# Kernel tuning notes

Hardware: AMD Instinct MI355X
Metric: run time of the kernel (lower is better)

Reference implementation:

```python
import jax, jax.numpy as jnp
import numpy as np

B, N, D = 4, 4096, 512
H = 8
HD = D // H  # 64


def setup_inputs() -> dict:
    key = jax.random.key(0)
    ks = jax.random.split(key, 9)
    s = 1.0 / np.sqrt(D)
    return {
        "x": jax.random.normal(ks[0], (B, N, D), dtype=jnp.float32),
        "Wq": jax.random.normal(ks[1], (D, D), dtype=jnp.float32) * s,
        "bq": jax.random.normal(ks[2], (D,), dtype=jnp.float32) * 0.01,
        "Wk": jax.random.normal(ks[3], (D, D), dtype=jnp.float32) * s,
        "bk": jax.random.normal(ks[4], (D,), dtype=jnp.float32) * 0.01,
        "Wv": jax.random.normal(ks[5], (D, D), dtype=jnp.float32) * s,
        "bv": jax.random.normal(ks[6], (D,), dtype=jnp.float32) * 0.01,
        "Wo": jax.random.normal(ks[7], (D, D), dtype=jnp.float32) * s,
        "bo": jax.random.normal(ks[8], (D,), dtype=jnp.float32) * 0.01,
    }


def reference(x, Wq, bq, Wk, bk, Wv, bv, Wo, bo):
    # projections -> [B, H, N, HD]
    def split_heads(t):
        return t.reshape(B, N, H, HD).transpose(0, 2, 1, 3)

    q = split_heads(x @ Wq.T + bq)
    k = split_heads(x @ Wk.T + bk)
    v = split_heads(x @ Wv.T + bv)

    scale = 1.0 / np.sqrt(HD).astype(np.float32)
    scores = jnp.einsum("bhqd,bhkd->bhqk", q, k) * scale  # [B,H,N,N]
    attn = jax.nn.softmax(scores, axis=-1)
    out = jnp.einsum("bhqk,bhkd->bhqd", attn, v)  # [B,H,N,HD]
    out = out.transpose(0, 2, 1, 3).reshape(B, N, D)
    return out @ Wo.T + bo
```

## Files before the change

kernel.cpp:

```cpp
#include <hip/hip_runtime.h>
#include <hip/hip_bf16.h>

#define BB 4
#define NN 4096
#define DD 512
#define HH 8
#define HD 64

typedef __attribute__((ext_vector_type(4))) float f32x4;
typedef __attribute__((ext_vector_type(16))) float f32x16;
typedef __attribute__((ext_vector_type(8))) short short8;
typedef __attribute__((ext_vector_type(4))) unsigned int uint4v;

static __device__ __forceinline__ unsigned short f2bf(float f) {
    unsigned int u = __float_as_uint(f);
    u += 0x7fff + ((u >> 16) & 1);
    return (unsigned short)(u >> 16);
}

__global__ void convert_bf16(const float* __restrict__ in,
                             unsigned short* __restrict__ out, int n) {
    int i = (blockIdx.x * blockDim.x + threadIdx.x) * 8;
    int stride = gridDim.x * blockDim.x * 8;
    for (; i + 7 < n; i += stride) {
        f32x4 a = *reinterpret_cast<const f32x4*>(in + i);
        f32x4 b = *reinterpret_cast<const f32x4*>(in + i + 4);
        short8 o;
        o[0] = (short)f2bf(a[0]); o[1] = (short)f2bf(a[1]);
        o[2] = (short)f2bf(a[2]); o[3] = (short)f2bf(a[3]);
        o[4] = (short)f2bf(b[0]); o[5] = (short)f2bf(b[1]);
        o[6] = (short)f2bf(b[2]); o[7] = (short)f2bf(b[3]);
        *reinterpret_cast<short8*>(out + i) = o;
    }
}

__global__ void convert_weights(const float* __restrict__ W0, const float* __restrict__ W1,
                                const float* __restrict__ W2, const float* __restrict__ W3,
                                unsigned short* __restrict__ out) {
    int which = blockIdx.x >> 7;
    const float* src = which == 0 ? W0 : which == 1 ? W1 : which == 2 ? W2 : W3;
    unsigned short* dst = out + (size_t)which * DD * DD;
    int i = ((blockIdx.x & 127) * blockDim.x + threadIdx.x) * 8;
    f32x4 a = *reinterpret_cast<const f32x4*>(src + i);
    f32x4 b = *reinterpret_cast<const f32x4*>(src + i + 4);
    short8 o;
    o[0] = (short)f2bf(a[0]); o[1] = (short)f2bf(a[1]);
    o[2] = (short)f2bf(a[2]); o[3] = (short)f2bf(a[3]);
    o[4] = (short)f2bf(b[0]); o[5] = (short)f2bf(b[1]);
    o[6] = (short)f2bf(b[2]); o[7] = (short)f2bf(b[3]);
    *reinterpret_cast<short8*>(dst + i) = o;
}

template <int OUT_BF16>
__global__ __launch_bounds__(256)
void gemm_bias(const unsigned short* __restrict__ A,
               const unsigned short* __restrict__ W,
               const float* __restrict__ bias,
               void* __restrict__ Cout, float scale) {
    __shared__ uint4 ldsA[128 * 4];
    __shared__ uint4 ldsB[128 * 4];
    const int t = threadIdx.x;
    const int lane = t & 63;
    const int w = t >> 6;
    const int wr = w >> 1, wc = w & 1;
    const int brow = (int)blockIdx.y * 128;
    const int bcol = (int)blockIdx.x * 128;
    const int l16 = lane & 15;
    const int lq = lane >> 4;

    f32x4 acc[4][4] = {};

    const int sr = t >> 1;
    const int c16 = (t & 1) * 2;

    for (int k0 = 0; k0 < 512; k0 += 32) {
        const uint4* gA = reinterpret_cast<const uint4*>(A + (size_t)(brow + sr) * 512 + k0 + c16 * 8);
        const uint4* gB = reinterpret_cast<const uint4*>(W + (size_t)(bcol + sr) * 512 + k0 + c16 * 8);
        uint4 a0 = gA[0], a1 = gA[1];
        uint4 b0 = gB[0], b1 = gB[1];
        __syncthreads();
        ldsA[(sr * 4 + c16) ^ (sr & 7)]     = a0;
        ldsA[(sr * 4 + c16 + 1) ^ (sr & 7)] = a1;
        ldsB[(sr * 4 + c16) ^ (sr & 7)]     = b0;
        ldsB[(sr * 4 + c16 + 1) ^ (sr & 7)] = b1;
        __syncthreads();
        short8 af[4], bfr[4];
#pragma unroll
        for (int m = 0; m < 4; ++m) {
            int ra = wr * 64 + m * 16 + l16;
            af[m] = *reinterpret_cast<short8*>(&ldsA[(ra * 4 + lq) ^ (ra & 7)]);
            int rb = wc * 64 + m * 16 + l16;
            bfr[m] = *reinterpret_cast<short8*>(&ldsB[(rb * 4 + lq) ^ (rb & 7)]);
        }
#pragma unroll
        for (int m = 0; m < 4; ++m)
#pragma unroll
            for (int n = 0; n < 4; ++n)
                acc[m][n] = __builtin_amdgcn_mfma_f32_16x16x32_bf16(af[m], bfr[n], acc[m][n], 0, 0, 0);
    }

#pragma unroll
    for (int m = 0; m < 4; ++m) {
        int row = brow + wr * 64 + m * 16 + lq * 4;
#pragma unroll
        for (int n = 0; n < 4; ++n) {
            int col = bcol + wc * 64 + n * 16 + l16;
            float bv = bias[col];
#pragma unroll
            for (int r = 0; r < 4; ++r) {
                float v = (acc[m][n][r] + bv) * scale;
                if (OUT_BF16) {
                    ((unsigned short*)Cout)[(size_t)(row + r) * 512 + col] = f2bf(v);
                } else {
                    ((float*)Cout)[(size_t)(row + r) * 512 + col] = v;
                }
            }
        }
    }
}

__global__ __launch_bounds__(256)
void transpose_v(const unsigned short* __restrict__ Vb, unsigned short* __restrict__ Vt) {
    __shared__ unsigned short tile[64][72];
    const int bh = blockIdx.y;
    const int b = bh >> 3, h = bh & 7;
    const int n0 = blockIdx.x * 64;
    const int t = threadIdx.x;
    {
        int r = t >> 2;
        int cs = (t & 3) * 16;
        const short8* src = reinterpret_cast<const short8*>(
            Vb + (size_t)(b * NN + n0 + r) * DD + h * HD + cs);
        short8 v0 = src[0], v1 = src[1];
#pragma unroll
        for (int j = 0; j < 8; ++j) {
            tile[r][cs + j]     = (unsigned short)v0[j];
            tile[r][cs + 8 + j] = (unsigned short)v1[j];
        }
    }
    __syncthreads();
    {
        int d = t >> 2;
        int ns = (t & 3) * 16;
        short8 o0, o1;
#pragma unroll
        for (int j = 0; j < 8; ++j) {
            o0[j] = (short)tile[ns + j][d];
            o1[j] = (short)tile[ns + 8 + j][d];
        }
        unsigned short* dst = Vt + ((size_t)bh * HD + d) * NN + n0 + ns;
        *reinterpret_cast<short8*>(dst)     = o0;
        *reinterpret_cast<short8*>(dst + 8) = o1;
    }
}

__global__ __launch_bounds__(256, 3)
void flash_attn(const unsigned short* __restrict__ Qb,
                const unsigned short* __restrict__ Kb,
                const unsigned short* __restrict__ Vt,
                unsigned short* __restrict__ Ob) {
    __shared__ __align__(16) char lds[32768];
    const int t = threadIdx.x;
    const int lane = t & 63;
    const int w = t >> 6;
    const int nid = (blockIdx.x & 7) * 128 + (blockIdx.x >> 3);
    const int bh = nid >> 5;
    const int qb = nid & 31;
    const int b = bh >> 3, h = bh & 7;
    const int q0 = qb * 128 + w * 32;
    const int l32 = lane & 31;
    const int hi = lane >> 5;

    const int i8 = lane >> 3, g8 = lane & 7;

    const unsigned short* qptr = Qb + (size_t)(b * NN + q0 + l32) * DD + h * HD + hi * 8;
    short8 qf[4];
#pragma unroll
    for (int c = 0; c < 4; ++c)
        qf[c] = *reinterpret_cast<const short8*>(qptr + c * 16);

    const f32x16 Z = {};
    f32x16 OT0 = {}, OT1 = {};
    float lsx = 0.f, lsy = 0.f;

    int koff[8], voff[8];
#pragma unroll
    for (int sub = 0; sub < 2; ++sub) {
#pragma unroll
        for (int c = 0; c < 4; ++c) {
            int row = sub * 32 + l32;
            int g = (hi + 2 * c) ^ (row & 7) ^ ((row >> 3) & 7);
            koff[sub * 4 + c] = row * 128 + g * 16;
        }
#pragma unroll
        for (int dblk = 0; dblk < 2; ++dblk)
#pragma unroll
            for (int c2 = 0; c2 < 2; ++c2) {
                int row = dblk * 32 + l32;
                int g = ((sub << 2) + (c2 << 1) + hi) ^ (row & 7) ^ ((row >> 3) & 7);
                voff[sub * 4 + dblk * 2 + c2] = 8192 + row * 128 + g * 16;
            }
    }

    const int rowl0 = w * 16 + i8;
    const int rowl1 = w * 16 + 8 + i8;
    const int gs0 = (g8 ^ i8 ^ ((2 * w) & 7)) * 8;
    const int gs1 = (g8 ^ i8 ^ ((2 * w + 1) & 7)) * 8;
    const unsigned short* kp0 = Kb + (size_t)(b * NN + rowl0) * DD + h * HD + gs0;
    const unsigned short* kp1 = Kb + (size_t)(b * NN + rowl1) * DD + h * HD + gs1;
    const unsigned short* vp0 = Vt + ((size_t)bh * HD + rowl0) * NN + gs0;
    const unsigned short* vp1 = Vt + ((size_t)bh * HD + rowl1) * NN + gs1;

    auto STAGE = [&](int bb) {
        __builtin_amdgcn_global_load_lds(
            (const __attribute__((address_space(1))) void*)kp0,
            (__attribute__((address_space(3))) void*)(lds + bb + (w * 16) * 128), 16, 0, 0);
        __builtin_amdgcn_global_load_lds(
            (const __attribute__((address_space(1))) void*)kp1,
            (__attribute__((address_space(3))) void*)(lds + bb + (w * 16 + 8) * 128), 16, 0, 0);
        __builtin_amdgcn_global_load_lds(
            (const __attribute__((address_space(1))) void*)vp0,
            (__attribute__((address_space(3))) void*)(lds + bb + 8192 + (w * 16) * 128), 16, 0, 0);
        __builtin_amdgcn_global_load_lds(
            (const __attribute__((address_space(1))) void*)vp1,
            (__attribute__((address_space(3))) void*)(lds + bb + 8192 + (w * 16 + 8) * 128), 16, 0, 0);
        kp0 += 64 * DD; kp1 += 64 * DD; vp0 += 64; vp1 += 64;
    };

    auto softpack = [&](const f32x16& S, short8& pa, short8& pb) {
        unsigned int wq[8];
#pragma unroll
        for (int j = 0; j < 8; ++j) {
            float p0 = __builtin_exp2f(S[2 * j]);
            float p1 = __builtin_exp2f(S[2 * j + 1]);
            lsx += p0; lsy += p1;
            asm("v_cvt_pk_bf16_f32 %0, %1, %2" : "=v"(wq[j]) : "v"(p0), "v"(p1));
        }
        asm("v_permlane32_swap_b32 %0, %1" : "+v"(wq[0]), "+v"(wq[2]));
        asm("v_permlane32_swap_b32 %0, %1" : "+v"(wq[1]), "+v"(wq[3]));
        asm("v_permlane32_swap_b32 %0, %1" : "+v"(wq[4]), "+v"(wq[6]));
        asm("v_permlane32_swap_b32 %0, %1" : "+v"(wq[5]), "+v"(wq[7]));
        uint4v pu0 = {wq[0], wq[1], wq[2], wq[3]};
        uint4v pu1 = {wq[4], wq[5], wq[6], wq[7]};
        pa = __builtin_bit_cast(short8, pu0);
        pb = __builtin_bit_cast(short8, pu1);
    };

    auto COMPUTE = [&](int BO) {
        short8 kf0, kf1, kf2, kf3;
        kf0 = *reinterpret_cast<const short8*>(lds + BO + koff[0]);
        kf1 = *reinterpret_cast<const short8*>(lds + BO + koff[1]);
        kf2 = *reinterpret_cast<const short8*>(lds + BO + koff[2]);
        kf3 = *reinterpret_cast<const short8*>(lds + BO + koff[3]);
        f32x16 S;
        __builtin_amdgcn_s_setprio(1);
        S = __builtin_amdgcn_mfma_f32_32x32x16_bf16(kf0, qf[0], Z, 0, 0, 0);
        S = __builtin_amdgcn_mfma_f32_32x32x16_bf16(kf1, qf[1], S, 0, 0, 0);
        S = __builtin_amdgcn_mfma_f32_32x32x16_bf16(kf2, qf[2], S, 0, 0, 0);
        S = __builtin_amdgcn_mfma_f32_32x32x16_bf16(kf3, qf[3], S, 0, 0, 0);
        __builtin_amdgcn_s_setprio(0);
        short8 vf0 = *reinterpret_cast<const short8*>(lds + BO + voff[0]);
        short8 vf1 = *reinterpret_cast<const short8*>(lds + BO + voff[1]);
        short8 vf2 = *reinterpret_cast<const short8*>(lds + BO + voff[2]);
        short8 vf3 = *reinterpret_cast<const short8*>(lds + BO + voff[3]);
        kf0 = *reinterpret_cast<const short8*>(lds + BO + koff[4]);
        kf1 = *reinterpret_cast<const short8*>(lds + BO + koff[5]);
        kf2 = *reinterpret_cast<const short8*>(lds + BO + koff[6]);
        kf3 = *reinterpret_cast<const short8*>(lds + BO + koff[7]);
        short8 pa, pb;
        softpack(S, pa, pb);
        __builtin_amdgcn_s_setprio(1);
        S = __builtin_amdgcn_mfma_f32_32x32x16_bf16(kf0, qf[0], Z, 0, 0, 0);
        S = __builtin_amdgcn_mfma_f32_32x32x16_bf16(kf1, qf[1], S, 0, 0, 0);
        OT0 = __builtin_amdgcn_mfma_f32_32x32x16_bf16(vf0, pa, OT0, 0, 0, 0);
        OT0 = __builtin_amdgcn_mfma_f32_32x32x16_bf16(vf1, pb, OT0, 0, 0, 0);
        S = __builtin_amdgcn_mfma_f32_32x32x16_bf16(kf2, qf[2], S, 0, 0, 0);
        S = __builtin_amdgcn_mfma_f32_32x32x16_bf16(kf3, qf[3], S, 0, 0, 0);
        OT1 = __builtin_amdgcn_mfma_f32_32x32x16_bf16(vf2, pa, OT1, 0, 0, 0);
        OT1 = __builtin_amdgcn_mfma_f32_32x32x16_bf16(vf3, pb, OT1, 0, 0, 0);
        __builtin_amdgcn_s_setprio(0);
        vf0 = *reinterpret_cast<const short8*>(lds + BO + voff[4]);
        vf1 = *reinterpret_cast<const short8*>(lds + BO + voff[5]);
        vf2 = *reinterpret_cast<const short8*>(lds + BO + voff[6]);
        vf3 = *reinterpret_cast<const short8*>(lds + BO + voff[7]);
        softpack(S, pa, pb);
        __builtin_amdgcn_s_setprio(1);
        OT0 = __builtin_amdgcn_mfma_f32_32x32x16_bf16(vf0, pa, OT0, 0, 0, 0);
        OT0 = __builtin_amdgcn_mfma_f32_32x32x16_bf16(vf1, pb, OT0, 0, 0, 0);
        OT1 = __builtin_amdgcn_mfma_f32_32x32x16_bf16(vf2, pa, OT1, 0, 0, 0);
        OT1 = __builtin_amdgcn_mfma_f32_32x32x16_bf16(vf3, pb, OT1, 0, 0, 0);
        __builtin_amdgcn_s_setprio(0);
    };

    STAGE(0);
    asm volatile("s_waitcnt vmcnt(0)" ::: "memory");
    __builtin_amdgcn_s_barrier();
    asm volatile("" ::: "memory");

    for (int it = 0; it < 32; ++it) {
        STAGE(16384);
        asm volatile("s_waitcnt vmcnt(4)" ::: "memory");
        __builtin_amdgcn_s_barrier();
        asm volatile("" ::: "memory");
        COMPUTE(0);
        asm volatile("" ::: "memory");
        __builtin_amdgcn_s_barrier();
        asm volatile("" ::: "memory");
        if (it != 31) {
            STAGE(0);
            asm volatile("s_waitcnt vmcnt(4)" ::: "memory");
        } else {
            asm volatile("s_waitcnt vmcnt(0)" ::: "memory");
        }
        __builtin_amdgcn_s_barrier();
        asm volatile("" ::: "memory");
        COMPUTE(16384);
        if (it != 31) {
            asm volatile("" ::: "memory");
            __builtin_amdgcn_s_barrier();
            asm volatile("" ::: "memory");
        }
    }

    float lsum = lsx + lsy;
    lsum += __shfl_xor(lsum, 32);
    float inv = 1.0f / lsum;
    char* lw = lds + w * 4096;
#pragma unroll
    for (int dblk = 0; dblk < 2; ++dblk) {
#pragma unroll
        for (int g = 0; g < 4; ++g) {
#pragma unroll
            for (int j = 0; j < 2; ++j) {
                int r = 4 * g + 2 * j;
                int d = dblk * 32 + 8 * g + 2 * j + 4 * hi;
                float a = (dblk ? OT1[r] : OT0[r]) * inv;
                float bqv = (dblk ? OT1[r + 1] : OT0[r + 1]) * inv;
                unsigned int wv;
                asm("v_cvt_pk_bf16_f32 %0, %1, %2" : "=v"(wv) : "v"(a), "v"(bqv));
                int addr = (l32 * 128 + d * 2) ^ ((l32 & 7) << 4);
                *reinterpret_cast<unsigned int*>(lw + addr) = wv;
            }
        }
    }
#pragma unroll
    for (int it = 0; it < 4; ++it) {
        int q = lane >> 1;
        int seg = (lane & 1) + it * 2;
        uint4 val = *reinterpret_cast<uint4*>(lw + ((q * 128 + seg * 16) ^ ((q & 7) << 4)));
        *reinterpret_cast<uint4*>(Ob + (size_t)(b * NN + q0 + q) * DD + h * HD + seg * 8) = val;
    }
}

extern "C" void kernel_launch(void* const* d_in, const int* in_sizes, int n_in,
                              void* d_out, int out_size, void* d_ws, size_t ws_size,
                              hipStream_t stream) {
    (void)in_sizes; (void)n_in; (void)out_size; (void)ws_size;
    const float* x  = (const float*)d_in[0];
    const float* Wq = (const float*)d_in[1];
    const float* bq = (const float*)d_in[2];
    const float* Wk = (const float*)d_in[3];
    const float* bk = (const float*)d_in[4];
    const float* Wv = (const float*)d_in[5];
    const float* bv = (const float*)d_in[6];
    const float* Wo = (const float*)d_in[7];
    const float* bo = (const float*)d_in[8];
    float* out = (float*)d_out;

    char* ws = (char*)d_ws;
    const size_t BUF = 16777216;
    unsigned short* xb  = (unsigned short*)(ws);
    unsigned short* Qb  = (unsigned short*)(ws + BUF);
    unsigned short* Kb  = (unsigned short*)(ws + 2 * BUF);
    unsigned short* Vb  = (unsigned short*)(ws + 3 * BUF);
    unsigned short* Wqb = (unsigned short*)(ws + 4 * BUF);
    unsigned short* Wkb = Wqb + 262144;
    unsigned short* Wvb = Wkb + 262144;
    unsigned short* Wob = Wvb + 262144;
    unsigned short* Vt  = xb;
    unsigned short* Ob  = Vb;

    const int NTOK = BB * NN;
    const float cl = 0.125f * 1.4426950408889634f;

    convert_bf16<<<2048, 256, 0, stream>>>(x, xb, NTOK * DD);
    convert_weights<<<512, 256, 0, stream>>>(Wq, Wk, Wv, Wo, Wqb);

    dim3 ggrid(4, NTOK / 128);
    gemm_bias<1><<<ggrid, 256, 0, stream>>>(xb, Wqb, bq, Qb, cl);
    gemm_bias<1><<<ggrid, 256, 0, stream>>>(xb, Wkb, bk, Kb, 1.0f);
    gemm_bias<1><<<ggrid, 256, 0, stream>>>(xb, Wvb, bv, Vb, 1.0f);

    transpose_v<<<dim3(NN / 64, BB * HH), 256, 0, stream>>>(Vb, Vt);

    flash_attn<<<1024, 256, 0, stream>>>(Qb, Kb, Vt, Ob);

    gemm_bias<0><<<ggrid, 256, 0, stream>>>(Ob, Wob, bo, out, 1.0f);
}
```

Measured before the change: 335.7 us.

## Merge QKV projection launches and simplify flash-attention inner loop schedule

Result: faster. 278.5 us (-17.0%).

```diff
diff --git a/kernel.cpp b/kernel.cpp
--- a/kernel.cpp
+++ b/kernel.cpp
@@ -52,19 +52,16 @@
 }
 
 template <int OUT_BF16>
-__global__ __launch_bounds__(256)
-void gemm_bias(const unsigned short* __restrict__ A,
+__device__ __forceinline__
+void gemm_tile(const unsigned short* __restrict__ A,
                const unsigned short* __restrict__ W,
                const float* __restrict__ bias,
-               void* __restrict__ Cout, float scale) {
-    __shared__ uint4 ldsA[128 * 4];
-    __shared__ uint4 ldsB[128 * 4];
+               void* __restrict__ Cout, float scale,
+               int brow, int bcol, uint4* ldsA, uint4* ldsB) {
     const int t = threadIdx.x;
     const int lane = t & 63;
     const int w = t >> 6;
     const int wr = w >> 1, wc = w & 1;
-    const int brow = (int)blockIdx.y * 128;
-    const int bcol = (int)blockIdx.x * 128;
     const int l16 = lane & 15;
     const int lq = lane >> 4;
 
@@ -117,6 +114,35 @@
             }
         }
     }
+}
+
+__global__ __launch_bounds__(256)
+void gemm_qkv(const unsigned short* __restrict__ xb,
+              const unsigned short* __restrict__ Wall,
+              const float* __restrict__ bq, const float* __restrict__ bk,
+              const float* __restrict__ bv,
+              unsigned short* __restrict__ Qb, unsigned short* __restrict__ Kb,
+              unsigned short* __restrict__ Vb, float cl) {
+    __shared__ uint4 ldsA[128 * 4];
+    __shared__ uint4 ldsB[128 * 4];
+    int z = blockIdx.z;
+    const unsigned short* W = Wall + (size_t)z * DD * DD;
+    const float* bias = z == 0 ? bq : z == 1 ? bk : bv;
+    unsigned short* dst = z == 0 ? Qb : z == 1 ? Kb : Vb;
+    float scale = z == 0 ? cl : 1.0f;
+    gemm_tile<1>(xb, W, bias, dst, scale,
+                 (int)blockIdx.y * 128, (int)blockIdx.x * 128, ldsA, ldsB);
+}
+
+__global__ __launch_bounds__(256)
+void gemm_bias_f32(const unsigned short* __restrict__ A,
+                   const unsigned short* __restrict__ W,
+                   const float* __restrict__ bias,
+                   float* __restrict__ Cout) {
+    __shared__ uint4 ldsA[128 * 4];
+    __shared__ uint4 ldsB[128 * 4];
+    gemm_tile<0>(A, W, bias, Cout, 1.0f,
+                 (int)blockIdx.y * 128, (int)blockIdx.x * 128, ldsA, ldsB);
 }
 
 __global__ __launch_bounds__(256)
@@ -181,7 +207,7 @@
 
     const f32x16 Z = {};
     f32x16 OT0 = {}, OT1 = {};
-    float lsx = 0.f, lsy = 0.f;
+    float lsum = 0.f;
 
     int koff[8], voff[8];
 #pragma unroll
@@ -233,7 +259,7 @@
         for (int j = 0; j < 8; ++j) {
             float p0 = __builtin_exp2f(S[2 * j]);
             float p1 = __builtin_exp2f(S[2 * j + 1]);
-            lsx += p0; lsy += p1;
+            lsum += p0 + p1;
             asm("v_cvt_pk_bf16_f32 %0, %1, %2" : "=v"(wq[j]) : "v"(p0), "v"(p1));
         }
         asm("v_permlane32_swap_b32 %0, %1" : "+v"(wq[0]), "+v"(wq[2]));
@@ -247,49 +273,28 @@
     };
 
     auto COMPUTE = [&](int BO) {
-        short8 kf0, kf1, kf2, kf3;
-        kf0 = *reinterpret_cast<const short8*>(lds + BO + koff[0]);
-        kf1 = *reinterpret_cast<const short8*>(lds + BO + koff[1]);
-        kf2 = *reinterpret_cast<const short8*>(lds + BO + koff[2]);
-        kf3 = *reinterpret_cast<const short8*>(lds + BO + koff[3]);
-        f32x16 S;
-        __builtin_amdgcn_s_setprio(1);
-        S = __builtin_amdgcn_mfma_f32_32x32x16_bf16(kf0, qf[0], Z, 0, 0, 0);
-        S = __builtin_amdgcn_mfma_f32_32x32x16_bf16(kf1, qf[1], S, 0, 0, 0);
-        S = __builtin_amdgcn_mfma_f32_32x32x16_bf16(kf2, qf[2], S, 0, 0, 0);
-        S = __builtin_amdgcn_mfma_f32_32x32x16_bf16(kf3, qf[3], S, 0, 0, 0);
-        __builtin_amdgcn_s_setprio(0);
-        short8 vf0 = *reinterpret_cast<const short8*>(lds + BO + voff[0]);
-        short8 vf1 = *reinterpret_cast<const short8*>(lds + BO + voff[1]);
-        short8 vf2 = *reinterpret_cast<const short8*>(lds + BO + voff[2]);
-        short8 vf3 = *reinterpret_cast<const short8*>(lds + BO + voff[3]);
-        kf0 = *reinterpret_cast<const short8*>(lds + BO + koff[4]);
-        kf1 = *reinterpret_cast<const short8*>(lds + BO + koff[5]);
-        kf2 = *reinterpret_cast<const short8*>(lds + BO + koff[6]);
-        kf3 = *reinterpret_cast<const short8*>(lds + BO + koff[7]);
-        short8 pa, pb;
-        softpack(S, pa, pb);
-        __builtin_amdgcn_s_setprio(1);
-        S = __builtin_amdgcn_mfma_f32_32x32x16_bf16(kf0, qf[0], Z, 0, 0, 0);
-        S = __builtin_amdgcn_mfma_f32_32x32x16_bf16(kf1, qf[1], S, 0, 0, 0);
-        OT0 = __builtin_amdgcn_mfma_f32_32x32x16_bf16(vf0, pa, OT0, 0, 0, 0);
-        OT0 = __builtin_amdgcn_mfma_f32_32x32x16_bf16(vf1, pb, OT0, 0, 0, 0);
-        S = __builtin_amdgcn_mfma_f32_32x32x16_bf16(kf2, qf[2], S, 0, 0, 0);
-        S = __builtin_amdgcn_mfma_f32_32x32x16_bf16(kf3, qf[3], S, 0, 0, 0);
-        OT1 = __builtin_amdgcn_mfma_f32_32x32x16_bf16(vf2, pa, OT1, 0, 0, 0);
-        OT1 = __builtin_amdgcn_mfma_f32_32x32x16_bf16(vf3, pb, OT1, 0, 0, 0);
-        __builtin_amdgcn_s_setprio(0);
-        vf0 = *reinterpret_cast<const short8*>(lds + BO + voff[4]);
-        vf1 = *reinterpret_cast<const short8*>(lds + BO + voff[5]);
-        vf2 = *reinterpret_cast<const short8*>(lds + BO + voff[6]);
-        vf3 = *reinterpret_cast<const short8*>(lds + BO + voff[7]);
-        softpack(S, pa, pb);
-        __builtin_amdgcn_s_setprio(1);
-        OT0 = __builtin_amdgcn_mfma_f32_32x32x16_bf16(vf0, pa, OT0, 0, 0, 0);
-        OT0 = __builtin_amdgcn_mfma_f32_32x32x16_bf16(vf1, pb, OT0, 0, 0, 0);
-        OT1 = __builtin_amdgcn_mfma_f32_32x32x16_bf16(vf2, pa, OT1, 0, 0, 0);
-        OT1 = __builtin_amdgcn_mfma_f32_32x32x16_bf16(vf3, pb, OT1, 0, 0, 0);
-        __builtin_amdgcn_s_setprio(0);
+#pragma unroll
+        for (int sub = 0; sub < 2; ++sub) {
+            short8 kf0 = *reinterpret_cast<const short8*>(lds + BO + koff[sub * 4 + 0]);
+            short8 kf1 = *reinterpret_cast<const short8*>(lds + BO + koff[sub * 4 + 1]);
+            short8 kf2 = *reinterpret_cast<const short8*>(lds + BO + koff[sub * 4 + 2]);
+            short8 kf3 = *reinterpret_cast<const short8*>(lds + BO + koff[sub * 4 + 3]);
+            f32x16 S;
+            S = __builtin_amdgcn_mfma_f32_32x32x16_bf16(kf0, qf[0], Z, 0, 0, 0);
+            S = __builtin_amdgcn_mfma_f32_32x32x16_bf16(kf1, qf[1], S, 0, 0, 0);
+            S = __builtin_amdgcn_mfma_f32_32x32x16_bf16(kf2, qf[2], S, 0, 0, 0);
+            S = __builtin_amdgcn_mfma_f32_32x32x16_bf16(kf3, qf[3], S, 0, 0, 0);
+            short8 vf0 = *reinterpret_cast<const short8*>(lds + BO + voff[sub * 4 + 0]);
+            short8 vf1 = *reinterpret_cast<const short8*>(lds + BO + voff[sub * 4 + 1]);
+            short8 vf2 = *reinterpret_cast<const short8*>(lds + BO + voff[sub * 4 + 2]);
+            short8 vf3 = *reinterpret_cast<const short8*>(lds + BO + voff[sub * 4 + 3]);
+            short8 pa, pb;
+            softpack(S, pa, pb);
+            OT0 = __builtin_amdgcn_mfma_f32_32x32x16_bf16(vf0, pa, OT0, 0, 0, 0);
+            OT0 = __builtin_amdgcn_mfma_f32_32x32x16_bf16(vf1, pb, OT0, 0, 0, 0);
+            OT1 = __builtin_amdgcn_mfma_f32_32x32x16_bf16(vf2, pa, OT1, 0, 0, 0);
+            OT1 = __builtin_amdgcn_mfma_f32_32x32x16_bf16(vf3, pb, OT1, 0, 0, 0);
+        }
     };
 
     STAGE(0);
@@ -322,7 +327,6 @@
         }
     }
 
-    float lsum = lsx + lsy;
     lsum += __shfl_xor(lsum, 32);
     float inv = 1.0f / lsum;
     char* lw = lds + w * 4096;
@@ -374,9 +378,7 @@
     unsigned short* Kb  = (unsigned short*)(ws + 2 * BUF);
     unsigned short* Vb  = (unsigned short*)(ws + 3 * BUF);
     unsigned short* Wqb = (unsigned short*)(ws + 4 * BUF);
-    unsigned short* Wkb = Wqb + 262144;
-    unsigned short* Wvb = Wkb + 262144;
-    unsigned short* Wob = Wvb + 262144;
+    unsigned short* Wob = Wqb + 3 * 262144;
     unsigned short* Vt  = xb;
     unsigned short* Ob  = Vb;
 
@@ -386,14 +388,12 @@
     convert_bf16<<<2048, 256, 0, stream>>>(x, xb, NTOK * DD);
     convert_weights<<<512, 256, 0, stream>>>(Wq, Wk, Wv, Wo, Wqb);
 
-    dim3 ggrid(4, NTOK / 128);
-    gemm_bias<1><<<ggrid, 256, 0, stream>>>(xb, Wqb, bq, Qb, cl);
-    gemm_bias<1><<<ggrid, 256, 0, stream>>>(xb, Wkb, bk, Kb, 1.0f);
-    gemm_bias<1><<<ggrid, 256, 0, stream>>>(xb, Wvb, bv, Vb, 1.0f);
+    dim3 ggrid(4, NTOK / 128, 3);
+    gemm_qkv<<<ggrid, 256, 0, stream>>>(xb, Wqb, bq, bk, bv, Qb, Kb, Vb, cl);
 
     transpose_v<<<dim3(NN / 64, BB * HH), 256, 0, stream>>>(Vb, Vt);
 
     flash_attn<<<1024, 256, 0, stream>>>(Qb, Kb, Vt, Ob);
 
-    gemm_bias<0><<<ggrid, 256, 0, stream>>>(Ob, Wob, bo, out, 1.0f);
-}
+    gemm_bias_f32<<<dim3(4, NTOK / 128), 256, 0, stream>>>(Ob, Wob, bo, out);
+}
```
